# Kernel tuning notes

Hardware: AMD Instinct MI355X
Metric: run time of the kernel (lower is better)

The kernel has to match this reference:

```python
import jax, jax.numpy as jnp
import numpy as np

VOCAB, DIM, N_LORA, RANK, T, NSEG = 32000, 2048, 9, 16, 8192, 16


def setup_inputs() -> dict:
    key = jax.random.key(0)
    ks = jax.random.split(key, 7)
    input_ids = jax.random.randint(ks[0], (T,), 0, VOCAB, dtype=jnp.int32)
    weight = jax.random.normal(ks[1], (VOCAB, DIM), dtype=jnp.float32) * 0.02
    A_buffer = jax.random.normal(ks[2], (N_LORA, VOCAB, RANK), dtype=jnp.float32) * 0.02
    B_buffer = jax.random.normal(ks[3], (N_LORA, DIM, RANK), dtype=jnp.float32) * 0.02
    interior = jnp.sort(jax.random.randint(ks[4], (NSEG - 1,), 0, T, dtype=jnp.int32))
    seg_indptr = jnp.concatenate([jnp.zeros((1,), jnp.int32), interior, jnp.full((1,), T, jnp.int32)])
    weight_indices = jax.random.randint(ks[5], (NSEG,), 0, N_LORA, dtype=jnp.int32)
    scalings = jax.random.uniform(ks[6], (N_LORA,), dtype=jnp.float32, minval=0.5, maxval=2.0)
    return {"input_ids": input_ids, "weight": weight, "A_buffer": A_buffer,
            "B_buffer": B_buffer, "seg_indptr": seg_indptr,
            "weight_indices": weight_indices, "scalings": scalings}


def reference(input_ids, weight, A_buffer, B_buffer, seg_indptr, weight_indices, scalings):
    # Base embedding gather: [T, DIM]
    base = weight[input_ids]
    T_ = input_ids.shape[0]
    # Map each token to its segment, then to its per-segment LoRA slot.
    seg_id = jnp.searchsorted(seg_indptr, jnp.arange(T_, dtype=seg_indptr.dtype), side='right') - 1
    w = weight_indices[seg_id]                      # [T] lora slot per token
    active = (w != 0).astype(base.dtype)            # slot 0 == no LoRA
    # Per-token LoRA A row gather: [T, RANK]
    a = A_buffer[w, input_ids]
    a = a * (scalings[w] * active)[:, None]
    # contrib[t] = B_buffer[w[t]] @ a[t]; route via one-hot over the small
    # lora axis to avoid materializing a [T, DIM, RANK] gather of B.
    oh = jax.nn.one_hot(w, B_buffer.shape[0], dtype=base.dtype)  # [T, L]
    contrib = jnp.einsum('tl,tr,ldr->td', oh, a, B_buffer)
    return base + contrib
```

## Files before the change

kernel.cpp:

```cpp
#include <hip/hip_runtime.h>

#define VOCAB 32000
#define DIM 2048
#define N_LORA 9
#define RANK 16
#define NSEG 16
#define TB 16
#define BLOCK 256

typedef float f32x4 __attribute__((ext_vector_type(4)));

struct Smem {
    int ids[TB];
    int w[TB];
    float scale[TB];
    f32x4 a[TB][RANK / 4];
};

__device__ __forceinline__ void token_body(
    int tk, int t0, int d,
    const Smem& s,
    const float* __restrict__ weight,
    const float* __restrict__ B_buffer,
    float* __restrict__ out,
    f32x4 (&b)[16], int& wcur)
{
    const int w = s.w[tk];
    if (w != wcur) {
        wcur = w;
        const f32x4* bp = reinterpret_cast<const f32x4*>(
            B_buffer + ((size_t)w * DIM + (size_t)d) * RANK);
        #pragma unroll
        for (int j = 0; j < 16; ++j) b[j] = bp[j];
    }
    const f32x4 a0 = s.a[tk][0], a1 = s.a[tk][1], a2 = s.a[tk][2], a3 = s.a[tk][3];
    const f32x4 wv = *reinterpret_cast<const f32x4*>(
        weight + (size_t)s.ids[tk] * DIM + d);
    f32x4 o;
    o.x = wv.x
        + b[ 0].x*a0.x + b[ 0].y*a0.y + b[ 0].z*a0.z + b[ 0].w*a0.w
        + b[ 1].x*a1.x + b[ 1].y*a1.y + b[ 1].z*a1.z + b[ 1].w*a1.w
        + b[ 2].x*a2.x + b[ 2].y*a2.y + b[ 2].z*a2.z + b[ 2].w*a2.w
        + b[ 3].x*a3.x + b[ 3].y*a3.y + b[ 3].z*a3.z + b[ 3].w*a3.w;
    o.y = wv.y
        + b[ 4].x*a0.x + b[ 4].y*a0.y + b[ 4].z*a0.z + b[ 4].w*a0.w
        + b[ 5].x*a1.x + b[ 5].y*a1.y + b[ 5].z*a1.z + b[ 5].w*a1.w
        + b[ 6].x*a2.x + b[ 6].y*a2.y + b[ 6].z*a2.z + b[ 6].w*a2.w
        + b[ 7].x*a3.x + b[ 7].y*a3.y + b[ 7].z*a3.z + b[ 7].w*a3.w;
    o.z = wv.z
        + b[ 8].x*a0.x + b[ 8].y*a0.y + b[ 8].z*a0.z + b[ 8].w*a0.w
        + b[ 9].x*a1.x + b[ 9].y*a1.y + b[ 9].z*a1.z + b[ 9].w*a1.w
        + b[10].x*a2.x + b[10].y*a2.y + b[10].z*a2.z + b[10].w*a2.w
        + b[11].x*a3.x + b[11].y*a3.y + b[11].z*a3.z + b[11].w*a3.w;
    o.w = wv.w
        + b[12].x*a0.x + b[12].y*a0.y + b[12].z*a0.z + b[12].w*a0.w
        + b[13].x*a1.x + b[13].y*a1.y + b[13].z*a1.z + b[13].w*a1.w
        + b[14].x*a2.x + b[14].y*a2.y + b[14].z*a2.z + b[14].w*a2.w
        + b[15].x*a3.x + b[15].y*a3.y + b[15].z*a3.z + b[15].w*a3.w;
    __builtin_nontemporal_store(o, reinterpret_cast<f32x4*>(
        out + (size_t)(t0 + tk) * DIM + d));
}

__global__ __launch_bounds__(BLOCK) void lora_embed_kernel(
    const int* __restrict__ input_ids,
    const float* __restrict__ weight,
    const float* __restrict__ A_buffer,
    const float* __restrict__ B_buffer,
    const int* __restrict__ seg_indptr,
    const int* __restrict__ weight_indices,
    const float* __restrict__ scalings,
    float* __restrict__ out,
    int T)
{
    __shared__ Smem s;

    const int tid = threadIdx.x;
    const int t0 = blockIdx.x * TB;

    if (tid < TB) {
        int tg = t0 + tid;
        int tc = tg < T ? tg : T - 1;
        int id = input_ids[tc];
        int seg = -1;
        #pragma unroll
        for (int i = 0; i < NSEG; ++i)
            seg += (seg_indptr[i] <= tc) ? 1 : 0;
        int w = weight_indices[seg];
        s.ids[tid] = id;
        s.w[tid] = w;
        s.scale[tid] = (w != 0) ? scalings[w] : 0.0f;
    }
    __syncthreads();

    if (tid < TB * 4) {
        const int t = tid >> 2, q = tid & 3;
        const f32x4* arow = reinterpret_cast<const f32x4*>(
            A_buffer + ((size_t)s.w[t] * VOCAB + (size_t)s.ids[t]) * RANK);
        f32x4 av = arow[q];
        s.a[t][q] = av * s.scale[t];
    }
    __syncthreads();

    const int d = (blockIdx.y * BLOCK + tid) * 4;

    f32x4 b[16];
    int wcur = -1;

    if (t0 + TB <= T) {
        #pragma unroll 4
        for (int t = 0; t < TB; ++t)
            token_body(t, t0, d, s, weight, B_buffer, out, b, wcur);
    } else {
        const int nt = T - t0;
        for (int t = 0; t < nt; ++t)
            token_body(t, t0, d, s, weight, B_buffer, out, b, wcur);
    }
}

extern "C" void kernel_launch(void* const* d_in, const int* in_sizes, int n_in,
                              void* d_out, int out_size, void* d_ws, size_t ws_size,
                              hipStream_t stream) {
    const int*   input_ids      = (const int*)d_in[0];
    const float* weight         = (const float*)d_in[1];
    const float* A_buffer       = (const float*)d_in[2];
    const float* B_buffer       = (const float*)d_in[3];
    const int*   seg_indptr     = (const int*)d_in[4];
    const int*   weight_indices = (const int*)d_in[5];
    const float* scalings       = (const float*)d_in[6];
    float* out = (float*)d_out;

    const int T = in_sizes[0];
    dim3 grid((T + TB - 1) / TB, DIM / (BLOCK * 4));
    lora_embed_kernel<<<grid, BLOCK, 0, stream>>>(
        input_ids, weight, A_buffer, B_buffer,
        seg_indptr, weight_indices, scalings, out, T);
}
```

Baseline: 36.95 us.

## Split LoRA A-row gather into a separate prep kernel writing workspace

Adds a prep kernel that computes each token's segment, LoRA slot and scaled A row once and writes them to workspace. The main kernel then loads precomputed slots and A values without the serial segment search and dependent A gather, which shortens the two-barrier prologue that the old version repeated in every DIM-split block. It also drops the nontemporal store in favor of a plain store and adds a minimum-blocks launch bound. The cost is a second kernel launch plus extra workspace reads and writes.

```diff
diff --git a/kernel.cpp b/kernel.cpp
--- a/kernel.cpp
+++ b/kernel.cpp
@@ -10,22 +10,46 @@
 
 typedef float f32x4 __attribute__((ext_vector_type(4)));
 
-struct Smem {
-    int ids[TB];
-    int w[TB];
-    float scale[TB];
-    f32x4 a[TB][RANK / 4];
-};
+__global__ void prep_kernel(
+    const int* __restrict__ input_ids,
+    const float* __restrict__ A_buffer,
+    const int* __restrict__ seg_indptr,
+    const int* __restrict__ weight_indices,
+    const float* __restrict__ scalings,
+    float* __restrict__ a_sc,
+    int* __restrict__ w_arr,
+    int T)
+{
+    const int g = blockIdx.x * blockDim.x + threadIdx.x;
+    const int t = g >> 2, q = g & 3;
+    if (t >= T) return;
+
+    const int id = input_ids[t];
+    int seg = -1;
+    #pragma unroll
+    for (int i = 0; i < NSEG; ++i)
+        seg += (seg_indptr[i] <= t) ? 1 : 0;
+    const int w = weight_indices[seg];
+    const float s = (w != 0) ? scalings[w] : 0.0f;
+    if (q == 0) w_arr[t] = w;
+
+    const f32x4* arow = reinterpret_cast<const f32x4*>(
+        A_buffer + ((size_t)w * VOCAB + (size_t)id) * RANK);
+    f32x4 av = arow[q] * s;
+    *reinterpret_cast<f32x4*>(a_sc + (size_t)t * RANK + q * 4) = av;
+}
 
 __device__ __forceinline__ void token_body(
     int tk, int t0, int d,
-    const Smem& s,
+    const int* __restrict__ ids_s,
+    const int* __restrict__ w_s,
+    const f32x4 (* __restrict__ a_s)[RANK / 4],
     const float* __restrict__ weight,
     const float* __restrict__ B_buffer,
     float* __restrict__ out,
     f32x4 (&b)[16], int& wcur)
 {
-    const int w = s.w[tk];
+    const int w = w_s[tk];
     if (w != wcur) {
         wcur = w;
         const f32x4* bp = reinterpret_cast<const f32x4*>(
@@ -33,9 +57,9 @@
         #pragma unroll
         for (int j = 0; j < 16; ++j) b[j] = bp[j];
     }
-    const f32x4 a0 = s.a[tk][0], a1 = s.a[tk][1], a2 = s.a[tk][2], a3 = s.a[tk][3];
+    const f32x4 a0 = a_s[tk][0], a1 = a_s[tk][1], a2 = a_s[tk][2], a3 = a_s[tk][3];
     const f32x4 wv = *reinterpret_cast<const f32x4*>(
-        weight + (size_t)s.ids[tk] * DIM + d);
+        weight + (size_t)ids_s[tk] * DIM + d);
     f32x4 o;
     o.x = wv.x
         + b[ 0].x*a0.x + b[ 0].y*a0.y + b[ 0].z*a0.z + b[ 0].w*a0.w
@@ -57,22 +81,21 @@
         + b[13].x*a1.x + b[13].y*a1.y + b[13].z*a1.z + b[13].w*a1.w
         + b[14].x*a2.x + b[14].y*a2.y + b[14].z*a2.z + b[14].w*a2.w
         + b[15].x*a3.x + b[15].y*a3.y + b[15].z*a3.z + b[15].w*a3.w;
-    __builtin_nontemporal_store(o, reinterpret_cast<f32x4*>(
-        out + (size_t)(t0 + tk) * DIM + d));
+    *reinterpret_cast<f32x4*>(out + (size_t)(t0 + tk) * DIM + d) = o;
 }
 
-__global__ __launch_bounds__(BLOCK) void lora_embed_kernel(
+__global__ __launch_bounds__(BLOCK, 4) void lora_embed_kernel(
     const int* __restrict__ input_ids,
     const float* __restrict__ weight,
-    const float* __restrict__ A_buffer,
     const float* __restrict__ B_buffer,
-    const int* __restrict__ seg_indptr,
-    const int* __restrict__ weight_indices,
-    const float* __restrict__ scalings,
+    const float* __restrict__ a_sc,
+    const int* __restrict__ w_arr,
     float* __restrict__ out,
     int T)
 {
-    __shared__ Smem s;
+    __shared__ int ids_s[TB];
+    __shared__ int w_s[TB];
+    __shared__ f32x4 a_s[TB][RANK / 4];
 
     const int tid = threadIdx.x;
     const int t0 = blockIdx.x * TB;
@@ -80,24 +103,13 @@
     if (tid < TB) {
         int tg = t0 + tid;
         int tc = tg < T ? tg : T - 1;
-        int id = input_ids[tc];
-        int seg = -1;
-        #pragma unroll
-        for (int i = 0; i < NSEG; ++i)
-            seg += (seg_indptr[i] <= tc) ? 1 : 0;
-        int w = weight_indices[seg];
-        s.ids[tid] = id;
-        s.w[tid] = w;
-        s.scale[tid] = (w != 0) ? scalings[w] : 0.0f;
+        ids_s[tid] = input_ids[tc];
+        w_s[tid] = w_arr[tc];
     }
-    __syncthreads();
-
-    if (tid < TB * 4) {
-        const int t = tid >> 2, q = tid & 3;
-        const f32x4* arow = reinterpret_cast<const f32x4*>(
-            A_buffer + ((size_t)s.w[t] * VOCAB + (size_t)s.ids[t]) * RANK);
-        f32x4 av = arow[q];
-        s.a[t][q] = av * s.scale[t];
+    {
+        size_t idx = (size_t)t0 * RANK + tid;
+        size_t cap = (size_t)T * RANK - 1;
+        reinterpret_cast<float*>(a_s)[tid] = a_sc[idx < cap ? idx : cap];
     }
     __syncthreads();
 
@@ -108,12 +120,12 @@
 
     if (t0 + TB <= T) {
         #pragma unroll 4
-        for (int t = 0; t < TB; ++t)
-            token_body(t, t0, d, s, weight, B_buffer, out, b, wcur);
+        for (int tk = 0; tk < TB; ++tk)
+            token_body(tk, t0, d, ids_s, w_s, a_s, weight, B_buffer, out, b, wcur);
     } else {
         const int nt = T - t0;
-        for (int t = 0; t < nt; ++t)
-            token_body(t, t0, d, s, weight, B_buffer, out, b, wcur);
+        for (int tk = 0; tk < nt; ++tk)
+            token_body(tk, t0, d, ids_s, w_s, a_s, weight, B_buffer, out, b, wcur);
     }
 }
 
@@ -130,8 +142,15 @@
     float* out = (float*)d_out;
 
     const int T = in_sizes[0];
+
+    float* a_sc  = (float*)d_ws;
+    int*   w_arr = (int*)((char*)d_ws + (size_t)T * RANK * sizeof(float));
+
+    prep_kernel<<<(T * 4 + BLOCK - 1) / BLOCK, BLOCK, 0, stream>>>(
+        input_ids, A_buffer, seg_indptr, weight_indices, scalings,
+        a_sc, w_arr, T);
+
     dim3 grid((T + TB - 1) / TB, DIM / (BLOCK * 4));
     lora_embed_kernel<<<grid, BLOCK, 0, stream>>>(
-        input_ids, weight, A_buffer, B_buffer,
-        seg_indptr, weight_indices, scalings, out, T);
+        input_ids, weight, B_buffer, a_sc, w_arr, out, T);
 }
```

New measurement: 98.70 us. 2.67x slower.
